# Optimization experiments

Measured on AMD Instinct MI355X. Metric: run time of the kernel, lower is better.

## Reference

```python
import jax, jax.numpy as jnp
import numpy as np

B, S, D, H = 4, 2048, 1024, 16
DK = D // H

def setup_inputs() -> dict:
    key = jax.random.key(0)
    ks = jax.random.split(key, 7)
    f = lambda k, shape: jax.random.normal(k, shape, dtype=jnp.float32)
    return {
        "query": f(ks[0], (B, S, D)),
        "key":   f(ks[1], (B, S, D)),
        "value": f(ks[2], (B, S, D)),
        "w_q": f(ks[3], (D, D)) * (D ** -0.5),
        "w_k": f(ks[4], (D, D)) * (D ** -0.5),
        "w_v": f(ks[5], (D, D)) * (D ** -0.5),
        "w_o": f(ks[6], (D, D)) * (D ** -0.5),
    }

def reference(query, key, value, w_q, w_k, w_v, w_o):
    # Linear layers: y = x @ W^T (torch nn.Linear convention), bias=False
    def split_heads(x):  # [B,S,D] -> [B,H,S,DK]
        return x.reshape(B, S, H, DK).transpose(0, 2, 1, 3)
    Q = split_heads(query @ w_q.T)
    K = split_heads(key @ w_k.T)
    V = split_heads(value @ w_v.T)
    scale = jnp.float32(1.0 / np.sqrt(DK))
    scores = jnp.einsum('bhqd,bhkd->bhqk', Q, K) * scale  # [B,H,Sq,Sk]
    attn = jax.nn.softmax(scores, axis=-1)
    out = jnp.einsum('bhqk,bhkd->bhqd', attn, V)  # [B,H,Sq,DK]
    out = out.transpose(0, 2, 1, 3).reshape(B, S, D)
    return out @ w_o.T
```

## Files before the change

kernel.cpp:

```cpp
#include <hip/hip_runtime.h>
#include <stdint.h>

#define NB 4
#define NS 2048
#define ND 1024
#define NH 16
#define NDK 64
#define NM (NB*NS)

typedef __attribute__((ext_vector_type(8))) short short8;
typedef __attribute__((ext_vector_type(8))) unsigned short ushort8v;
typedef __attribute__((ext_vector_type(4))) unsigned short ushort4v;
typedef __attribute__((ext_vector_type(4))) float f32x4;
typedef __attribute__((ext_vector_type(16))) float f32x16;

__device__ __forceinline__ unsigned short f2bf(float f) {
  union { float f; uint32_t u; } v; v.f = f;
  uint32_t u = v.u;
  return (unsigned short)((u + 0x7FFFu + ((u >> 16) & 1u)) >> 16);
}

__device__ __forceinline__ void gload16(const void* g, void* l) {
  __builtin_amdgcn_global_load_lds(
      (const __attribute__((address_space(1))) void*)g,
      (__attribute__((address_space(3))) void*)l, 16, 0, 0);
}

__device__ __forceinline__ int xcd_swz(int flat, int nwg) {
  return (flat & 7) * (nwg >> 3) + (flat >> 3);
}

__global__ void convert_all(
    const float* __restrict__ x0, const float* __restrict__ x1, const float* __restrict__ x2,
    const float* __restrict__ w0, const float* __restrict__ w1,
    const float* __restrict__ w2, const float* __restrict__ w3,
    unsigned short* __restrict__ ox0, unsigned short* __restrict__ ox1, unsigned short* __restrict__ ox2,
    unsigned short* __restrict__ ow0, unsigned short* __restrict__ ow1,
    unsigned short* __restrict__ ow2, unsigned short* __restrict__ ow3)
{
  const float* src;
  unsigned short* dst;
  size_t i;
  if (blockIdx.y < 3) {
    src = blockIdx.y == 0 ? x0 : (blockIdx.y == 1 ? x1 : x2);
    dst = blockIdx.y == 0 ? ox0 : (blockIdx.y == 1 ? ox1 : ox2);
    i = ((size_t)blockIdx.x * 256 + threadIdx.x) * 8;
  } else {
    if (blockIdx.x >= 2048) return;
    size_t e = ((size_t)blockIdx.x * 256 + threadIdx.x) * 8;
    int which = (int)(e >> 20);
    size_t off = e & ((1u << 20) - 1);
    const float* ws[4] = {w0, w1, w2, w3};
    unsigned short* wd[4] = {ow0, ow1, ow2, ow3};
    src = ws[which]; dst = wd[which]; i = off;
  }
  f32x4 a = *(const f32x4*)(src + i);
  f32x4 b = *(const f32x4*)(src + i + 4);
  ushort8v h;
  h[0]=f2bf(a.x); h[1]=f2bf(a.y); h[2]=f2bf(a.z); h[3]=f2bf(a.w);
  h[4]=f2bf(b.x); h[5]=f2bf(b.y); h[6]=f2bf(b.z); h[7]=f2bf(b.w);
  *(ushort8v*)(dst + i) = h;
}

#define GPHASE(MH, NH, LA, LB)                                                 \
  {                                                                            \
    if (LA) {                                                                  \
      _Pragma("unroll") for (int mm = 0; mm < 4; ++mm)                         \
        _Pragma("unroll") for (int kk = 0; kk < 2; ++kk)                       \
          af[mm][kk] = *(const short8*)(Ab + (MH)*8192 + mm*2048 + rowb + aoff[kk]); \
    }                                                                          \
    if (LB) {                                                                  \
      _Pragma("unroll") for (int nn = 0; nn < NN; ++nn)                        \
        _Pragma("unroll") for (int kk = 0; kk < 2; ++kk)                       \
          bf[nn][kk] = *(const short8*)(Bb + (NH)*(NN*2048) + nn*2048 + rowb + aoff[kk]); \
    }                                                                          \
    __builtin_amdgcn_s_barrier();                                              \
    __builtin_amdgcn_s_setprio(1);                                             \
    _Pragma("unroll") for (int mm = 0; mm < 4; ++mm)                           \
      _Pragma("unroll") for (int nn = 0; nn < NN; ++nn)                        \
        _Pragma("unroll") for (int kk = 0; kk < 2; ++kk)                       \
          acc[(MH)*4+mm][(NH)*NN+nn] = __builtin_amdgcn_mfma_f32_16x16x32_bf16( \
              af[mm][kk], bf[nn][kk], acc[(MH)*4+mm][(NH)*NN+nn], 0, 0, 0);    \
    __builtin_amdgcn_s_setprio(0);                                             \
    __builtin_amdgcn_s_barrier();                                              \
  }

template<int OUT, int PRESCALE, int BN>
__device__ __forceinline__ void gemm256_core(
    const unsigned short* __restrict__ A,
    const unsigned short* __restrict__ Bt,
    void* __restrict__ Cout,
    unsigned short* lds, int m0, int n0)
{
  const int K = ND, N = ND;
  const int NN = BN / 128;
  const int NBL = BN / 64;
  const int ASZ = 16384, BSZ = BN * 64, SZ = ASZ + BSZ;
  const int tid = threadIdx.x;
  const int lane = tid & 63, wid = tid >> 6;
  const int l15 = lane & 15, lg = lane >> 4;
  const int wr = wid >> 2, wc = wid & 3;
  const float QSC = 0.125f * 1.44269504088896f;

  const unsigned short* Asrc[4];
  const unsigned short* Bsrc[NBL];
#pragma unroll
  for (int l = 0; l < 4; ++l) {
    int cidx = l*512 + tid;
    int r = cidx >> 3;
    int cs = ((cidx & 7) ^ (r & 7)) * 8;
    Asrc[l] = A + (size_t)(m0 + r)*K + cs;
  }
#pragma unroll
  for (int l = 0; l < NBL; ++l) {
    int cidx = l*512 + tid;
    int r = cidx >> 3;
    int cs = ((cidx & 7) ^ (r & 7)) * 8;
    Bsrc[l] = Bt + (size_t)(n0 + r)*K + cs;
  }

  const int rowb = l15 * 128;
  int aoff[2];
  aoff[0] = ((lg)     ^ (l15 & 7)) * 16;
  aoff[1] = ((4 + lg) ^ (l15 & 7)) * 16;

  f32x4 acc[8][2*NN] = {};
  short8 af[4][2], bf[NN][2];

#pragma unroll
  for (int l = 0; l < 4; ++l) gload16(Asrc[l], lds + l*4096 + tid*8);
#pragma unroll
  for (int l = 0; l < NBL; ++l) gload16(Bsrc[l], lds + ASZ + l*4096 + tid*8);
  asm volatile("s_waitcnt vmcnt(0)" ::: "memory");
  __builtin_amdgcn_s_barrier();

  const int NT = K / 64;
  for (int t = 0; t < NT; ++t) {
    const int cur = t & 1;
    if (t + 1 < NT) {
      unsigned short* dst = lds + (cur^1)*SZ;
#pragma unroll
      for (int l = 0; l < 4; ++l) gload16(Asrc[l] + (t+1)*64, dst + l*4096 + tid*8);
#pragma unroll
      for (int l = 0; l < NBL; ++l) gload16(Bsrc[l] + (t+1)*64, dst + ASZ + l*4096 + tid*8);
    }
    const char* Ab = (const char*)(lds + cur*SZ) + wr*16384;
    const char* Bb = (const char*)(lds + cur*SZ + ASZ) + wc*(BN*32);

    GPHASE(0, 0, 1, 1)
    GPHASE(0, 1, 0, 1)
    GPHASE(1, 1, 1, 0)
    GPHASE(1, 0, 0, 1)

    asm volatile("s_waitcnt vmcnt(0)" ::: "memory");
    __builtin_amdgcn_s_barrier();
  }

#pragma unroll
  for (int m = 0; m < 8; ++m)
#pragma unroll
    for (int n = 0; n < 2*NN; ++n)
#pragma unroll
      for (int i = 0; i < 4; ++i) {
        int row = m0 + wr*128 + m*16 + lg*4 + i;
        int col = n0 + wc*(BN/4) + n*16 + l15;
        float val = PRESCALE ? acc[m][n][i] * QSC : acc[m][n][i];
        if (OUT == 0)
          ((float*)Cout)[(size_t)row * N + col] = val;
        else if (OUT == 1)
          ((unsigned short*)Cout)[(size_t)row * N + col] = f2bf(val);
        else
          ((unsigned short*)Cout)[((size_t)((row >> 11)*1024 + col))*NS + (row & (NS-1))]
              = f2bf(val);
      }
}

__global__ __launch_bounds__(512, 2) void gemm_qkv(
    const unsigned short* __restrict__ Xq, const unsigned short* __restrict__ Wq, unsigned short* Qb,
    const unsigned short* __restrict__ Xk, const unsigned short* __restrict__ Wk, unsigned short* Kb,
    const unsigned short* __restrict__ Xv, const unsigned short* __restrict__ Wv, unsigned short* VbT)
{
  __shared__ unsigned short lds[65536];
  int flat = (blockIdx.z * 32 + blockIdx.y) * 4 + blockIdx.x;
  int swz = xcd_swz(flat, 384);
  int z = swz >> 7, rem = swz & 127;
  int m0 = (rem >> 2) * 256, n0 = (rem & 3) * 256;
  if (z == 0)      gemm256_core<1,1,256>(Xq, Wq, Qb,  lds, m0, n0);
  else if (z == 1) gemm256_core<1,0,256>(Xk, Wk, Kb,  lds, m0, n0);
  else             gemm256_core<2,0,256>(Xv, Wv, VbT, lds, m0, n0);
}

__global__ __launch_bounds__(512, 2) void gemm_o(
    const unsigned short* __restrict__ A, const unsigned short* __restrict__ Bt, float* C)
{
  __shared__ unsigned short lds[49152];
  int flat = blockIdx.y * 8 + blockIdx.x;
  int swz = xcd_swz(flat, 256);
  gemm256_core<0,0,128>(A, Bt, C, lds, (swz >> 3) * 256, (swz & 7) * 128);
}

__global__ __launch_bounds__(256, 2) void flash_attn(
    const unsigned short* __restrict__ Qb,
    const unsigned short* __restrict__ Kb,
    const unsigned short* __restrict__ VT,
    unsigned short* __restrict__ O)
{
  __shared__ unsigned short Kt[2][64*64];
  __shared__ unsigned short Vt[2][64*64];
  const int tid = threadIdx.x, lane = tid & 63, wid = tid >> 6;
  const int l31 = lane & 31, hi = lane >> 5;
  int flat = blockIdx.y * 8 + blockIdx.x;
  int swz = xcd_swz(flat, 512);
  const int bh = swz >> 3, b = bh >> 4, h = bh & 15;
  const int q0 = (swz & 7) * 256 + wid * 64;

  const unsigned short* Kp[2]; const unsigned short* Vp[2]; int dofs[2];
#pragma unroll
  for (int p = 0; p < 2; ++p) {
    int slot = tid + p*256;
    int g = slot >> 6, r = slot & 63;
    Kp[p] = Kb + ((size_t)(b*NS + r))*ND + h*64 + g*8;
    Vp[p] = VT + ((size_t)(bh*64 + r))*NS + g*8;
    dofs[p] = slot * 8;
  }

  short8 qf[2][4];
#pragma unroll
  for (int qs = 0; qs < 2; ++qs)
#pragma unroll
    for (int ks = 0; ks < 4; ++ks)
      qf[qs][ks] = *(const short8*)(Qb + (size_t)(b*NS + q0 + qs*32 + l31)*ND + h*64 + ks*16 + hi*8);

  f32x16 oacc[2][2] = {};
  float lsum[2] = {0.f, 0.f};

#pragma unroll
  for (int p = 0; p < 2; ++p) {
    gload16(Kp[p], &Kt[0][dofs[p]]);
    gload16(Vp[p], &Vt[0][dofs[p]]);
  }
  __syncthreads();

  for (int t = 0; t < NS/64; ++t) {
    const int cur = t & 1;
    if (t + 1 < NS/64) {
#pragma unroll
      for (int p = 0; p < 2; ++p) {
        gload16(Kp[p] + (size_t)(t+1)*64*ND, &Kt[cur^1][dofs[p]]);
        gload16(Vp[p] + (t+1)*64,            &Vt[cur^1][dofs[p]]);
      }
    }
    const char* Kc = (const char*)Kt[cur];
    const char* Vc = (const char*)Vt[cur];

    short8 pa[2][2][2];
    float rs[2] = {0.f, 0.f};

#pragma unroll
    for (int n = 0; n < 2; ++n) {
      f32x16 st[2] = {};
      const int r = n*32 + l31;
      __builtin_amdgcn_s_setprio(1);
#pragma unroll
      for (int ks = 0; ks < 4; ++ks) {
        short8 kf = *(const short8*)(Kc + (((2*ks + hi) << 10) + r*16));
        st[0] = __builtin_amdgcn_mfma_f32_32x32x16_bf16(kf, qf[0][ks], st[0], 0, 0, 0);
        st[1] = __builtin_amdgcn_mfma_f32_32x32x16_bf16(kf, qf[1][ks], st[1], 0, 0, 0);
      }
      __builtin_amdgcn_s_setprio(0);
#pragma unroll
      for (int qs = 0; qs < 2; ++qs) {
        float lrs = 0.f;
#pragma unroll
        for (int e = 0; e < 16; ++e) {
          float p = __builtin_amdgcn_exp2f(st[qs][e]);
          st[qs][e] = p;
          lrs += p;
        }
        rs[qs] += lrs;
        uint32_t w[4][2];
#pragma unroll
        for (int e = 0; e < 4; ++e) {
          asm("v_cvt_pk_bf16_f32 %0, %1, %2"
              : "=v"(w[e][0]) : "v"(st[qs][4*e+0]), "v"(st[qs][4*e+1]));
          asm("v_cvt_pk_bf16_f32 %0, %1, %2"
              : "=v"(w[e][1]) : "v"(st[qs][4*e+2]), "v"(st[qs][4*e+3]));
        }
#pragma unroll
        for (int ksl = 0; ksl < 2; ++ksl) {
          uint32_t a0 = w[2*ksl][0], b0 = w[2*ksl+1][0];
          uint32_t a1 = w[2*ksl][1], b1 = w[2*ksl+1][1];
          asm("v_permlane32_swap_b32 %0, %1" : "+v"(a0), "+v"(b0));
          asm("v_permlane32_swap_b32 %0, %1" : "+v"(a1), "+v"(b1));
          union { uint32_t u[4]; short8 s; } f;
          f.u[0] = a0; f.u[1] = a1; f.u[2] = b0; f.u[3] = b1;
          pa[qs][n][ksl] = f.s;
        }
      }
    }
#pragma unroll
    for (int qs = 0; qs < 2; ++qs) {
      rs[qs] += __shfl_xor(rs[qs], 32);
      lsum[qs] += rs[qs];
    }

    __builtin_amdgcn_s_setprio(1);
#pragma unroll
    for (int d = 0; d < 2; ++d) {
      const int dr = d*32 + l31;
#pragma unroll
      for (int n = 0; n < 2; ++n)
#pragma unroll
        for (int ksl = 0; ksl < 2; ++ksl) {
          const int g = n*4 + ksl*2 + hi;
          short8 vf = *(const short8*)(Vc + ((g << 10) + dr*16));
          oacc[0][d] = __builtin_amdgcn_mfma_f32_32x32x16_bf16(pa[0][n][ksl], vf, oacc[0][d], 0, 0, 0);
          oacc[1][d] = __builtin_amdgcn_mfma_f32_32x32x16_bf16(pa[1][n][ksl], vf, oacc[1][d], 0, 0, 0);
        }
    }
    __builtin_amdgcn_s_setprio(0);
    __syncthreads();
  }

#pragma unroll
  for (int qs = 0; qs < 2; ++qs) {
    float linv[16];
#pragma unroll
    for (int r = 0; r < 16; ++r)
      linv[r] = 1.0f / __shfl(lsum[qs], (r & 3) + 8*(r >> 2) + 4*hi);
#pragma unroll
    for (int d = 0; d < 2; ++d)
#pragma unroll
      for (int r = 0; r < 16; ++r) {
        int qrow = q0 + qs*32 + (r & 3) + 8*(r >> 2) + 4*hi;
        O[(size_t)(b*NS + qrow)*ND + h*64 + d*32 + l31] = f2bf(oacc[qs][d][r] * linv[r]);
      }
  }
}

extern "C" void kernel_launch(void* const* d_in, const int* in_sizes, int n_in,
                              void* d_out, int out_size, void* d_ws, size_t ws_size,
                              hipStream_t stream) {
  const float* q  = (const float*)d_in[0];
  const float* k  = (const float*)d_in[1];
  const float* v  = (const float*)d_in[2];
  const float* wq = (const float*)d_in[3];
  const float* wk = (const float*)d_in[4];
  const float* wv = (const float*)d_in[5];
  const float* wo = (const float*)d_in[6];

  unsigned short* Wq = (unsigned short*)d_ws;
  unsigned short* Wk = Wq + (size_t)ND*ND;
  unsigned short* Wv = Wk + (size_t)ND*ND;
  unsigned short* Wo = Wv + (size_t)ND*ND;
  unsigned short* Xq = Wo + (size_t)ND*ND;
  unsigned short* Xk = Xq + (size_t)NM*ND;
  unsigned short* Xv = Xk + (size_t)NM*ND;
  unsigned short* Qb = Xv + (size_t)NM*ND;
  unsigned short* Kb = Qb + (size_t)NM*ND;
  unsigned short* VbT = (unsigned short*)d_out;
  unsigned short* Ob  = Xq;

  convert_all<<<dim3(NM*ND/(256*8), 4), 256, 0, stream>>>(
      q, k, v, wq, wk, wv, wo, Xq, Xk, Xv, Wq, Wk, Wv, Wo);

  gemm_qkv<<<dim3(4, 32, 3), 512, 0, stream>>>(Xq, Wq, Qb, Xk, Wk, Kb, Xv, Wv, VbT);

  flash_attn<<<dim3(8, 64), 256, 0, stream>>>(Qb, Kb, VbT, Ob);

  gemm_o<<<dim3(8, 32), 512, 0, stream>>>(Ob, Wo, (float*)d_out);
}
```

Before: 205.7 us.

## Split flash attention key range across two wave groups per block

Each flash-attention block now runs 8 waves in two groups of four. Each group streams its own half of the keys through separate double-buffered LDS tiles. At the end, the partial row sums and output accumulators from group 1 are passed through LDS and added into group 0 before normalising and writing out. The aim is to double the resident waves and halve the serial key loop per wave, giving better latency hiding. In exchange it adds an LDS reduction epilogue with extra barriers, and the tighter launch bound may limit registers and cause spills.

```diff
diff --git a/kernel.cpp b/kernel.cpp
--- a/kernel.cpp
+++ b/kernel.cpp
@@ -199,28 +199,30 @@
   gemm256_core<0,0,128>(A, Bt, C, lds, (swz >> 3) * 256, (swz & 7) * 128);
 }
 
-__global__ __launch_bounds__(256, 2) void flash_attn(
+__global__ __launch_bounds__(512, 4) void flash_attn(
     const unsigned short* __restrict__ Qb,
     const unsigned short* __restrict__ Kb,
     const unsigned short* __restrict__ VT,
     unsigned short* __restrict__ O)
 {
-  __shared__ unsigned short Kt[2][64*64];
-  __shared__ unsigned short Vt[2][64*64];
+  __shared__ unsigned short Kt[2][2][64*64];
+  __shared__ unsigned short Vt[2][2][64*64];
   const int tid = threadIdx.x, lane = tid & 63, wid = tid >> 6;
   const int l31 = lane & 31, hi = lane >> 5;
+  const int grp = wid >> 2, widl = wid & 3;
+  const int ltid = tid & 255;
   int flat = blockIdx.y * 8 + blockIdx.x;
   int swz = xcd_swz(flat, 512);
   const int bh = swz >> 3, b = bh >> 4, h = bh & 15;
-  const int q0 = (swz & 7) * 256 + wid * 64;
+  const int q0 = (swz & 7) * 256 + widl * 64;
 
   const unsigned short* Kp[2]; const unsigned short* Vp[2]; int dofs[2];
 #pragma unroll
   for (int p = 0; p < 2; ++p) {
-    int slot = tid + p*256;
+    int slot = ltid + p*256;
     int g = slot >> 6, r = slot & 63;
-    Kp[p] = Kb + ((size_t)(b*NS + r))*ND + h*64 + g*8;
-    Vp[p] = VT + ((size_t)(bh*64 + r))*NS + g*8;
+    Kp[p] = Kb + ((size_t)(b*NS + grp*1024 + r))*ND + h*64 + g*8;
+    Vp[p] = VT + ((size_t)(bh*64 + r))*NS + grp*1024 + g*8;
     dofs[p] = slot * 8;
   }
 
@@ -234,24 +236,27 @@
   f32x16 oacc[2][2] = {};
   float lsum[2] = {0.f, 0.f};
 
+  unsigned short* Ktg = &Kt[grp][0][0];
+  unsigned short* Vtg = &Vt[grp][0][0];
+
 #pragma unroll
   for (int p = 0; p < 2; ++p) {
-    gload16(Kp[p], &Kt[0][dofs[p]]);
-    gload16(Vp[p], &Vt[0][dofs[p]]);
+    gload16(Kp[p], Ktg + dofs[p]);
+    gload16(Vp[p], Vtg + dofs[p]);
   }
   __syncthreads();
 
-  for (int t = 0; t < NS/64; ++t) {
+  for (int t = 0; t < 16; ++t) {
     const int cur = t & 1;
-    if (t + 1 < NS/64) {
+    if (t + 1 < 16) {
 #pragma unroll
       for (int p = 0; p < 2; ++p) {
-        gload16(Kp[p] + (size_t)(t+1)*64*ND, &Kt[cur^1][dofs[p]]);
-        gload16(Vp[p] + (t+1)*64,            &Vt[cur^1][dofs[p]]);
-      }
-    }
-    const char* Kc = (const char*)Kt[cur];
-    const char* Vc = (const char*)Vt[cur];
+        gload16(Kp[p] + (size_t)(t+1)*64*ND, Ktg + (cur^1)*4096 + dofs[p]);
+        gload16(Vp[p] + (t+1)*64,            Vtg + (cur^1)*4096 + dofs[p]);
+      }
+    }
+    const char* Kc = (const char*)(Ktg + cur*4096);
+    const char* Vc = (const char*)(Vtg + cur*4096);
 
     short8 pa[2][2][2];
     float rs[2] = {0.f, 0.f};
@@ -322,19 +327,39 @@
     __syncthreads();
   }
 
-#pragma unroll
-  for (int qs = 0; qs < 2; ++qs) {
-    float linv[16];
-#pragma unroll
-    for (int r = 0; r < 16; ++r)
-      linv[r] = 1.0f / __shfl(lsum[qs], (r & 3) + 8*(r >> 2) + 4*hi);
-#pragma unroll
-    for (int d = 0; d < 2; ++d)
-#pragma unroll
-      for (int r = 0; r < 16; ++r) {
-        int qrow = q0 + qs*32 + (r & 3) + 8*(r >> 2) + 4*hi;
-        O[(size_t)(b*NS + qrow)*ND + h*64 + d*32 + l31] = f2bf(oacc[qs][d][r] * linv[r]);
-      }
+  float* lsq = (float*)&Vt[0][0][0];
+  if (grp == 1) {
+    lsq[(widl*64 + lane)*2 + 0] = lsum[0];
+    lsq[(widl*64 + lane)*2 + 1] = lsum[1];
+  }
+  __syncthreads();
+  if (grp == 0) {
+    lsum[0] += lsq[(widl*64 + lane)*2 + 0];
+    lsum[1] += lsq[(widl*64 + lane)*2 + 1];
+  }
+
+  f32x16* obuf = (f32x16*)&Kt[0][0][0];
+#pragma unroll
+  for (int d = 0; d < 2; ++d) {
+    if (grp == 1) {
+      obuf[(widl*64 + lane)*2 + 0] = oacc[0][d];
+      obuf[(widl*64 + lane)*2 + 1] = oacc[1][d];
+    }
+    __syncthreads();
+    if (grp == 0) {
+#pragma unroll
+      for (int qs = 0; qs < 2; ++qs) {
+        f32x16 o2 = obuf[(widl*64 + lane)*2 + qs];
+#pragma unroll
+        for (int r = 0; r < 16; ++r) {
+          float li = 1.0f / __shfl(lsum[qs], (r & 3) + 8*(r >> 2) + 4*hi);
+          int qrow = q0 + qs*32 + (r & 3) + 8*(r >> 2) + 4*hi;
+          O[(size_t)(b*NS + qrow)*ND + h*64 + d*32 + l31]
+              = f2bf((oacc[qs][d][r] + o2[r]) * li);
+        }
+      }
+    }
+    __syncthreads();
   }
 }
 
@@ -366,7 +391,7 @@
 
   gemm_qkv<<<dim3(4, 32, 3), 512, 0, stream>>>(Xq, Wq, Qb, Xk, Wk, Kb, Xv, Wv, VbT);
 
-  flash_attn<<<dim3(8, 64), 256, 0, stream>>>(Qb, Kb, VbT, Ob);
+  flash_attn<<<dim3(8, 64), 512, 0, stream>>>(Qb, Kb, VbT, Ob);
 
   gemm_o<<<dim3(8, 32), 512, 0, stream>>>(Ob, Wo, (float*)d_out);
 }
```

Result: slower. 425.6 us (+106.9%).

## Triple-buffer K/V tiles in flash attention with partial vmcnt waits

Applied to the files above, without the earlier changes.

The K/V LDS staging in the flash attention kernel grows from two buffers to three, so tile t+2 is prefetched while tile t is computed. The full __syncthreads is replaced by s_waitcnt vmcnt(4) plus a raw s_barrier, so each wave waits only for the older loads and keeps the newest prefetch in flight. This hides more global-load latency. In exchange LDS use rises from 32KB to 48KB per block, which may limit occupancy at 2 blocks per CU, and correctness depends on the hand-set vmcnt count.

```diff
diff --git a/kernel.cpp b/kernel.cpp
--- a/kernel.cpp
+++ b/kernel.cpp
@@ -205,8 +205,8 @@
     const unsigned short* __restrict__ VT,
     unsigned short* __restrict__ O)
 {
-  __shared__ unsigned short Kt[2][64*64];
-  __shared__ unsigned short Vt[2][64*64];
+  __shared__ unsigned short Kt[3][64*64];
+  __shared__ unsigned short Vt[3][64*64];
   const int tid = threadIdx.x, lane = tid & 63, wid = tid >> 6;
   const int l31 = lane & 31, hi = lane >> 5;
   int flat = blockIdx.y * 8 + blockIdx.x;
@@ -234,28 +234,19 @@
   f32x16 oacc[2][2] = {};
   float lsum[2] = {0.f, 0.f};
 
-#pragma unroll
-  for (int p = 0; p < 2; ++p) {
-    gload16(Kp[p], &Kt[0][dofs[p]]);
-    gload16(Vp[p], &Vt[0][dofs[p]]);
-  }
-  __syncthreads();
-
-  for (int t = 0; t < NS/64; ++t) {
-    const int cur = t & 1;
-    if (t + 1 < NS/64) {
-#pragma unroll
-      for (int p = 0; p < 2; ++p) {
-        gload16(Kp[p] + (size_t)(t+1)*64*ND, &Kt[cur^1][dofs[p]]);
-        gload16(Vp[p] + (t+1)*64,            &Vt[cur^1][dofs[p]]);
-      }
-    }
-    const char* Kc = (const char*)Kt[cur];
-    const char* Vc = (const char*)Vt[cur];
-
+  auto stage = [&](int t, int bu) {
+#pragma unroll
+    for (int p = 0; p < 2; ++p) {
+      gload16(Kp[p] + (size_t)t*64*ND, &Kt[bu][dofs[p]]);
+      gload16(Vp[p] + t*64,            &Vt[bu][dofs[p]]);
+    }
+  };
+
+  auto tile = [&](int bu) {
+    const char* Kc = (const char*)&Kt[bu][0];
+    const char* Vc = (const char*)&Vt[bu][0];
     short8 pa[2][2][2];
     float rs[2] = {0.f, 0.f};
-
 #pragma unroll
     for (int n = 0; n < 2; ++n) {
       f32x16 st[2] = {};
@@ -319,8 +310,27 @@
         }
     }
     __builtin_amdgcn_s_setprio(0);
-    __syncthreads();
-  }
+  };
+
+  stage(0, 0);
+  stage(1, 1);
+  asm volatile("s_waitcnt vmcnt(4)" ::: "memory");
+  __builtin_amdgcn_s_barrier();
+
+  int bu = 0;
+  for (int t = 0; t < 30; ++t) {
+    int nb = bu + 2; if (nb >= 3) nb -= 3;
+    stage(t + 2, nb);
+    tile(bu);
+    asm volatile("s_waitcnt vmcnt(4)" ::: "memory");
+    __builtin_amdgcn_s_barrier();
+    bu = (bu + 1 == 3) ? 0 : bu + 1;
+  }
+  tile(bu);
+  asm volatile("s_waitcnt vmcnt(0)" ::: "memory");
+  __builtin_amdgcn_s_barrier();
+  bu = (bu + 1 == 3) ? 0 : bu + 1;
+  tile(bu);
 
 #pragma unroll
   for (int qs = 0; qs < 2; ++qs) {
```

New measurement: 207.3 us. Within noise of the previous version (+0.8%).

## Fuse fp32-to-bf16 conversion into GEMM loads and drop the convert kernel

Applied to the files above, without the earlier changes.

Removes the standalone convert_all kernel. The QKV and output-projection GEMMs now load fp32 activations and weights straight into registers, convert them to bf16 with packed cvt instructions, and write them into LDS in the middle of the MFMA phases, so staging overlaps compute. This drops a full bf16 round trip through memory and one launch. The cost is double the global read bytes per tile, register staging in place of direct global-to-LDS loads, and launch bounds lowered to one block per CU, which may reduce occupancy. Weights are also re-converted by every tile that reads them.

```diff
diff --git a/kernel.cpp b/kernel.cpp
--- a/kernel.cpp
+++ b/kernel.cpp
@@ -10,9 +10,10 @@
 
 typedef __attribute__((ext_vector_type(8))) short short8;
 typedef __attribute__((ext_vector_type(8))) unsigned short ushort8v;
-typedef __attribute__((ext_vector_type(4))) unsigned short ushort4v;
 typedef __attribute__((ext_vector_type(4))) float f32x4;
 typedef __attribute__((ext_vector_type(16))) float f32x16;
+
+typedef struct { uint32_t u[4]; } u32x4s;
 
 __device__ __forceinline__ unsigned short f2bf(float f) {
   union { float f; uint32_t u; } v; v.f = f;
@@ -20,6 +21,12 @@
   return (unsigned short)((u + 0x7FFFu + ((u >> 16) & 1u)) >> 16);
 }
 
+__device__ __forceinline__ uint32_t cvtpk(float lo, float hi) {
+  uint32_t r;
+  asm("v_cvt_pk_bf16_f32 %0, %1, %2" : "=v"(r) : "v"(lo), "v"(hi));
+  return r;
+}
+
 __device__ __forceinline__ void gload16(const void* g, void* l) {
   __builtin_amdgcn_global_load_lds(
       (const __attribute__((address_space(1))) void*)g,
@@ -28,38 +35,6 @@
 
 __device__ __forceinline__ int xcd_swz(int flat, int nwg) {
   return (flat & 7) * (nwg >> 3) + (flat >> 3);
-}
-
-__global__ void convert_all(
-    const float* __restrict__ x0, const float* __restrict__ x1, const float* __restrict__ x2,
-    const float* __restrict__ w0, const float* __restrict__ w1,
-    const float* __restrict__ w2, const float* __restrict__ w3,
-    unsigned short* __restrict__ ox0, unsigned short* __restrict__ ox1, unsigned short* __restrict__ ox2,
-    unsigned short* __restrict__ ow0, unsigned short* __restrict__ ow1,
-    unsigned short* __restrict__ ow2, unsigned short* __restrict__ ow3)
-{
-  const float* src;
-  unsigned short* dst;
-  size_t i;
-  if (blockIdx.y < 3) {
-    src = blockIdx.y == 0 ? x0 : (blockIdx.y == 1 ? x1 : x2);
-    dst = blockIdx.y == 0 ? ox0 : (blockIdx.y == 1 ? ox1 : ox2);
-    i = ((size_t)blockIdx.x * 256 + threadIdx.x) * 8;
-  } else {
-    if (blockIdx.x >= 2048) return;
-    size_t e = ((size_t)blockIdx.x * 256 + threadIdx.x) * 8;
-    int which = (int)(e >> 20);
-    size_t off = e & ((1u << 20) - 1);
-    const float* ws[4] = {w0, w1, w2, w3};
-    unsigned short* wd[4] = {ow0, ow1, ow2, ow3};
-    src = ws[which]; dst = wd[which]; i = off;
-  }
-  f32x4 a = *(const f32x4*)(src + i);
-  f32x4 b = *(const f32x4*)(src + i + 4);
-  ushort8v h;
-  h[0]=f2bf(a.x); h[1]=f2bf(a.y); h[2]=f2bf(a.z); h[3]=f2bf(a.w);
-  h[4]=f2bf(b.x); h[5]=f2bf(b.y); h[6]=f2bf(b.z); h[7]=f2bf(b.w);
-  *(ushort8v*)(dst + i) = h;
 }
 
 #define GPHASE(MH, NH, LA, LB)                                                 \
@@ -85,15 +60,16 @@
     __builtin_amdgcn_s_barrier();                                              \
   }
 
-template<int OUT, int PRESCALE, int BN>
+template<int OUT, int PRESCALE, int BN, int A32, int B32>
 __device__ __forceinline__ void gemm256_core(
-    const unsigned short* __restrict__ A,
-    const unsigned short* __restrict__ Bt,
+    const void* __restrict__ Ap,
+    const void* __restrict__ Btp,
     void* __restrict__ Cout,
     unsigned short* lds, int m0, int n0)
 {
   const int K = ND, N = ND;
   const int NN = BN / 128;
+  const int NAL = 4;
   const int NBL = BN / 64;
   const int ASZ = 16384, BSZ = BN * 64, SZ = ASZ + BSZ;
   const int tid = threadIdx.x;
@@ -102,21 +78,20 @@
   const int wr = wid >> 2, wc = wid & 3;
   const float QSC = 0.125f * 1.44269504088896f;
 
-  const unsigned short* Asrc[4];
-  const unsigned short* Bsrc[NBL];
-#pragma unroll
-  for (int l = 0; l < 4; ++l) {
+  size_t aofs[NAL], bofs[NBL];
+#pragma unroll
+  for (int l = 0; l < NAL; ++l) {
     int cidx = l*512 + tid;
     int r = cidx >> 3;
     int cs = ((cidx & 7) ^ (r & 7)) * 8;
-    Asrc[l] = A + (size_t)(m0 + r)*K + cs;
+    aofs[l] = (size_t)(m0 + r)*K + cs;
   }
 #pragma unroll
   for (int l = 0; l < NBL; ++l) {
     int cidx = l*512 + tid;
     int r = cidx >> 3;
     int cs = ((cidx & 7) ^ (r & 7)) * 8;
-    Bsrc[l] = Bt + (size_t)(n0 + r)*K + cs;
+    bofs[l] = (size_t)(n0 + r)*K + cs;
   }
 
   const int rowb = l15 * 128;
@@ -127,22 +102,65 @@
   f32x4 acc[8][2*NN] = {};
   short8 af[4][2], bf[NN][2];
 
-#pragma unroll
-  for (int l = 0; l < 4; ++l) gload16(Asrc[l], lds + l*4096 + tid*8);
-#pragma unroll
-  for (int l = 0; l < NBL; ++l) gload16(Bsrc[l], lds + ASZ + l*4096 + tid*8);
-  asm volatile("s_waitcnt vmcnt(0)" ::: "memory");
+  f32x4 sa[NAL][2], sb[NBL][2];
+
+#pragma unroll
+  for (int l = 0; l < NAL; ++l) {
+    if (A32) {
+      const float* s = (const float*)Ap + aofs[l];
+      sa[l][0] = *(const f32x4*)s; sa[l][1] = *(const f32x4*)(s + 4);
+    } else
+      gload16((const unsigned short*)Ap + aofs[l], lds + l*4096 + tid*8);
+  }
+#pragma unroll
+  for (int l = 0; l < NBL; ++l) {
+    if (B32) {
+      const float* s = (const float*)Btp + bofs[l];
+      sb[l][0] = *(const f32x4*)s; sb[l][1] = *(const f32x4*)(s + 4);
+    } else
+      gload16((const unsigned short*)Btp + bofs[l], lds + ASZ + l*4096 + tid*8);
+  }
+  if (A32) {
+#pragma unroll
+    for (int l = 0; l < NAL; ++l) {
+      u32x4s h = { cvtpk(sa[l][0].x, sa[l][0].y), cvtpk(sa[l][0].z, sa[l][0].w),
+                   cvtpk(sa[l][1].x, sa[l][1].y), cvtpk(sa[l][1].z, sa[l][1].w) };
+      *(u32x4s*)(lds + l*4096 + tid*8) = h;
+    }
+  }
+  if (B32) {
+#pragma unroll
+    for (int l = 0; l < NBL; ++l) {
+      u32x4s h = { cvtpk(sb[l][0].x, sb[l][0].y), cvtpk(sb[l][0].z, sb[l][0].w),
+                   cvtpk(sb[l][1].x, sb[l][1].y), cvtpk(sb[l][1].z, sb[l][1].w) };
+      *(u32x4s*)(lds + ASZ + l*4096 + tid*8) = h;
+    }
+  }
+  asm volatile("s_waitcnt vmcnt(0) lgkmcnt(0)" ::: "memory");
   __builtin_amdgcn_s_barrier();
 
   const int NT = K / 64;
   for (int t = 0; t < NT; ++t) {
     const int cur = t & 1;
+    unsigned short* dst = lds + (cur^1)*SZ;
     if (t + 1 < NT) {
-      unsigned short* dst = lds + (cur^1)*SZ;
-#pragma unroll
-      for (int l = 0; l < 4; ++l) gload16(Asrc[l] + (t+1)*64, dst + l*4096 + tid*8);
-#pragma unroll
-      for (int l = 0; l < NBL; ++l) gload16(Bsrc[l] + (t+1)*64, dst + ASZ + l*4096 + tid*8);
+      const int ko = (t+1)*64;
+#pragma unroll
+      for (int l = 0; l < NAL; ++l) {
+        if (A32) {
+          const float* s = (const float*)Ap + aofs[l] + ko;
+          sa[l][0] = *(const f32x4*)s; sa[l][1] = *(const f32x4*)(s + 4);
+        } else
+          gload16((const unsigned short*)Ap + aofs[l] + ko, dst + l*4096 + tid*8);
+      }
+#pragma unroll
+      for (int l = 0; l < NBL; ++l) {
+        if (B32) {
+          const float* s = (const float*)Btp + bofs[l] + ko;
+          sb[l][0] = *(const f32x4*)s; sb[l][1] = *(const f32x4*)(s + 4);
+        } else
+          gload16((const unsigned short*)Btp + bofs[l] + ko, dst + ASZ + l*4096 + tid*8);
+      }
     }
     const char* Ab = (const char*)(lds + cur*SZ) + wr*16384;
     const char* Bb = (const char*)(lds + cur*SZ + ASZ) + wc*(BN*32);
@@ -150,9 +168,27 @@
     GPHASE(0, 0, 1, 1)
     GPHASE(0, 1, 0, 1)
     GPHASE(1, 1, 1, 0)
+
+    if (A32 && t + 1 < NT) {
+#pragma unroll
+      for (int l = 0; l < NAL; ++l) {
+        u32x4s h = { cvtpk(sa[l][0].x, sa[l][0].y), cvtpk(sa[l][0].z, sa[l][0].w),
+                     cvtpk(sa[l][1].x, sa[l][1].y), cvtpk(sa[l][1].z, sa[l][1].w) };
+        *(u32x4s*)(dst + l*4096 + tid*8) = h;
+      }
+    }
+
     GPHASE(1, 0, 0, 1)
 
-    asm volatile("s_waitcnt vmcnt(0)" ::: "memory");
+    if (B32 && t + 1 < NT) {
+#pragma unroll
+      for (int l = 0; l < NBL; ++l) {
+        u32x4s h = { cvtpk(sb[l][0].x, sb[l][0].y), cvtpk(sb[l][0].z, sb[l][0].w),
+                     cvtpk(sb[l][1].x, sb[l][1].y), cvtpk(sb[l][1].z, sb[l][1].w) };
+        *(u32x4s*)(dst + ASZ + l*4096 + tid*8) = h;
+      }
+    }
+    asm volatile("s_waitcnt vmcnt(0) lgkmcnt(0)" ::: "memory");
     __builtin_amdgcn_s_barrier();
   }
 
@@ -175,28 +211,28 @@
       }
 }
 
-__global__ __launch_bounds__(512, 2) void gemm_qkv(
-    const unsigned short* __restrict__ Xq, const unsigned short* __restrict__ Wq, unsigned short* Qb,
-    const unsigned short* __restrict__ Xk, const unsigned short* __restrict__ Wk, unsigned short* Kb,
-    const unsigned short* __restrict__ Xv, const unsigned short* __restrict__ Wv, unsigned short* VbT)
+__global__ __launch_bounds__(512, 1) void gemm_qkv(
+    const float* __restrict__ Xq, const float* __restrict__ Wq, unsigned short* Qb,
+    const float* __restrict__ Xk, const float* __restrict__ Wk, unsigned short* Kb,
+    const float* __restrict__ Xv, const float* __restrict__ Wv, unsigned short* VbT)
 {
   __shared__ unsigned short lds[65536];
   int flat = (blockIdx.z * 32 + blockIdx.y) * 4 + blockIdx.x;
   int swz = xcd_swz(flat, 384);
   int z = swz >> 7, rem = swz & 127;
   int m0 = (rem >> 2) * 256, n0 = (rem & 3) * 256;
-  if (z == 0)      gemm256_core<1,1,256>(Xq, Wq, Qb,  lds, m0, n0);
-  else if (z == 1) gemm256_core<1,0,256>(Xk, Wk, Kb,  lds, m0, n0);
-  else             gemm256_core<2,0,256>(Xv, Wv, VbT, lds, m0, n0);
-}
-
-__global__ __launch_bounds__(512, 2) void gemm_o(
-    const unsigned short* __restrict__ A, const unsigned short* __restrict__ Bt, float* C)
+  if (z == 0)      gemm256_core<1,1,256,1,1>(Xq, Wq, Qb,  lds, m0, n0);
+  else if (z == 1) gemm256_core<1,0,256,1,1>(Xk, Wk, Kb,  lds, m0, n0);
+  else             gemm256_core<2,0,256,1,1>(Xv, Wv, VbT, lds, m0, n0);
+}
+
+__global__ __launch_bounds__(512, 1) void gemm_o(
+    const unsigned short* __restrict__ A, const float* __restrict__ Bt, float* C)
 {
   __shared__ unsigned short lds[49152];
   int flat = blockIdx.y * 8 + blockIdx.x;
   int swz = xcd_swz(flat, 256);
-  gemm256_core<0,0,128>(A, Bt, C, lds, (swz >> 3) * 256, (swz & 7) * 128);
+  gemm256_core<0,0,128,0,1>(A, Bt, C, lds, (swz >> 3) * 256, (swz & 7) * 128);
 }
 
 __global__ __launch_bounds__(256, 2) void flash_attn(
@@ -281,10 +317,8 @@
         uint32_t w[4][2];
 #pragma unroll
         for (int e = 0; e < 4; ++e) {
-          asm("v_cvt_pk_bf16_f32 %0, %1, %2"
-              : "=v"(w[e][0]) : "v"(st[qs][4*e+0]), "v"(st[qs][4*e+1]));
-          asm("v_cvt_pk_bf16_f32 %0, %1, %2"
-              : "=v"(w[e][1]) : "v"(st[qs][4*e+2]), "v"(st[qs][4*e+3]));
+          w[e][0] = cvtpk(st[qs][4*e+0], st[qs][4*e+1]);
+          w[e][1] = cvtpk(st[qs][4*e+2], st[qs][4*e+3]);
         }
 #pragma unroll
         for (int ksl = 0; ksl < 2; ++ksl) {
@@ -349,24 +383,14 @@
   const float* wv = (const float*)d_in[5];
   const float* wo = (const float*)d_in[6];
 
-  unsigned short* Wq = (unsigned short*)d_ws;
-  unsigned short* Wk = Wq + (size_t)ND*ND;
-  unsigned short* Wv = Wk + (size_t)ND*ND;
-  unsigned short* Wo = Wv + (size_t)ND*ND;
-  unsigned short* Xq = Wo + (size_t)ND*ND;
-  unsigned short* Xk = Xq + (size_t)NM*ND;
-  unsigned short* Xv = Xk + (size_t)NM*ND;
-  unsigned short* Qb = Xv + (size_t)NM*ND;
+  unsigned short* Qb = (unsigned short*)d_ws;
   unsigned short* Kb = Qb + (size_t)NM*ND;
+  unsigned short* Ob = Kb + (size_t)NM*ND;
   unsigned short* VbT = (unsigned short*)d_out;
-  unsigned short* Ob  = Xq;
-
-  convert_all<<<dim3(NM*ND/(256*8), 4), 256, 0, stream>>>(
-      q, k, v, wq, wk, wv, wo, Xq, Xk, Xv, Wq, Wk, Wv, Wo);
-
-  gemm_qkv<<<dim3(4, 32, 3), 512, 0, stream>>>(Xq, Wq, Qb, Xk, Wk, Kb, Xv, Wv, VbT);
+
+  gemm_qkv<<<dim3(4, 32, 3), 512, 0, stream>>>(q, wq, Qb, k, wk, Kb, v, wv, VbT);
 
   flash_attn<<<dim3(8, 64), 256, 0, stream>>>(Qb, Kb, VbT, Ob);
 
-  gemm_o<<<dim3(8, 32), 512, 0, stream>>>(Ob, Wo, (float*)d_out);
-}
+  gemm_o<<<dim3(8, 32), 512, 0, stream>>>(Ob, wo, (float*)d_out);
+}
```

Result: slower. 246.1 us (+19.6%).
